# Optimization experiments

Measured on AMD Instinct MI355X. Metric: run time of the kernel, lower is better.

The kernel has to match this reference:

```python
import jax, jax.numpy as jnp
import numpy as np

P = 4  # polynomial kernel degree


def setup_inputs() -> dict:
    key = jax.random.key(0)
    k1, k2, k3, k4 = jax.random.split(key, 4)
    m, n, d = 16384, 8192, 64
    x_p = jax.random.normal(k1, (m, d), dtype=jnp.float32)
    X = jax.random.normal(k2, (n, d), dtype=jnp.float32)
    alpha = jax.random.uniform(k3, (n,), dtype=jnp.float32, minval=0.0, maxval=0.2)
    b = jax.random.uniform(k4, (1,), dtype=jnp.float32, minval=0.0, maxval=0.2)
    return {"x_p": x_p, "X": X, "alpha": alpha, "b": b}


def reference(x_p, X, alpha, b):
    # SVR prediction with polynomial kernel, vectorized:
    # f(x_p) = sum_i alpha_i * (1 + x_p . X_i)^P + b
    # x_p: [m, d], X: [n, d] -> K: [m, n]
    K = (1.0 + jnp.einsum('md,nd->mn', x_p, X)) ** P
    return K @ alpha + b  # [m]
```

## Files before the change

kernel.cpp:

```cpp
#include <hip/hip_runtime.h>
#include <hip/hip_bf16.h>
#include <stdint.h>


typedef __attribute__((ext_vector_type(8))) short bf16x8;
typedef __attribute__((ext_vector_type(8))) unsigned short ushort8;
typedef __attribute__((ext_vector_type(4))) float f32x4;

#define MM 16384
#define NN 8192
#define DD 64
#define NSPLIT 8
#define CHUNK 64
#define CHUNKS_PER_BLK 16
#define BM 128

__device__ __forceinline__ unsigned short f2bf(float f) {
    uint32_t u = __float_as_uint(f);
    uint32_t r = (u + 0x7FFFu + ((u >> 16) & 1u)) >> 16;
    return (unsigned short)r;
}

__device__ __forceinline__ void gll16(const void* g, void* l) {
    __builtin_amdgcn_global_load_lds(
        (const __attribute__((address_space(1))) unsigned int*)g,
        (__attribute__((address_space(3))) unsigned int*)l, 16, 0, 0);
}

__global__ void convert_kernel(const float* __restrict__ xp,
                               const float* __restrict__ X,
                               const float* __restrict__ alpha,
                               unsigned short* __restrict__ xbf,
                               unsigned short* __restrict__ Xs,
                               float* __restrict__ alpha4f) {
    const int xp4 = MM * DD / 4;
    const int xu = NN * DD / 8;
    const int tot = xp4 + xu;
    int tid0 = blockIdx.x * blockDim.x + threadIdx.x;
    if (tid0 < NN) alpha4f[tid0] = sqrtf(sqrtf(alpha[tid0]));
    int stride = gridDim.x * blockDim.x;
    for (int i = tid0; i < tot; i += stride) {
        if (i < xp4) {
            float4 v = ((const float4*)xp)[i];
            ushort4 o;
            o.x = f2bf(v.x); o.y = f2bf(v.y); o.z = f2bf(v.z); o.w = f2bf(v.w);
            *(ushort4*)(xbf + (size_t)i * 4) = o;
        } else {
            int u = i - xp4;
            int n = u >> 3;
            int slot = u & 7;
            float a4 = sqrtf(sqrtf(alpha[n]));
            float4 va = ((const float4*)X)[n * 16 + slot * 2];
            float4 vb = ((const float4*)X)[n * 16 + slot * 2 + 1];
            ushort8 o;
            o[0] = f2bf(va.x * a4); o[1] = f2bf(va.y * a4);
            o[2] = f2bf(va.z * a4); o[3] = f2bf(va.w * a4);
            o[4] = f2bf(vb.x * a4); o[5] = f2bf(vb.y * a4);
            o[6] = f2bf(vb.z * a4); o[7] = f2bf(vb.w * a4);
            size_t dst = (size_t)(n >> 6) * 4096 + (n & 63) * 64
                       + ((slot ^ (n & 7)) * 8);
            *(ushort8*)(Xs + dst) = o;
        }
    }
}

__global__ __launch_bounds__(256) void svr_main(
        const unsigned short* __restrict__ xbf,
        const unsigned short* __restrict__ Xs,
        const float* __restrict__ alpha4f,
        float* __restrict__ partials) {
    __shared__ char smem[16384];
    const int tid  = threadIdx.x;
    const int lane = tid & 63;
    const int w    = tid >> 6;
    const int r    = lane & 15;
    const int g    = lane >> 4;
    const int mgroup = blockIdx.x >> 3;
    const int ns     = blockIdx.x & 7;

    bf16x8 a[2][2];
#pragma unroll
    for (int mt = 0; mt < 2; ++mt)
#pragma unroll
        for (int ks = 0; ks < 2; ++ks)
            a[mt][ks] = *(const bf16x8*)(
                xbf + (size_t)(mgroup * BM + w * 32 + mt * 16 + r) * DD
                    + ks * 32 + g * 8);

    f32x4 red[2];
#pragma unroll
    for (int mt = 0; mt < 2; ++mt) red[mt] = (f32x4){0.f, 0.f, 0.f, 0.f};

    const int chunk0 = ns * CHUNKS_PER_BLK;

    {
        const char* gs = (const char*)Xs + (size_t)chunk0 * 8192 + tid * 16;
        char* lb = smem + w * 1024;
        gll16(gs, lb);
        gll16(gs + 4096, lb + 4096);
    }
    float av4[4];
#pragma unroll
    for (int nt = 0; nt < 4; ++nt)
        av4[nt] = alpha4f[chunk0 * CHUNK + nt * 16 + r];
    __syncthreads();

    int cur = 0;
#pragma unroll 1
    for (int c = 0; c < CHUNKS_PER_BLK; ++c) {
        float av4n[4];
        if (c + 1 < CHUNKS_PER_BLK) {
            const char* gs = (const char*)Xs
                           + (size_t)(chunk0 + c + 1) * 8192 + tid * 16;
            char* lb = smem + (cur ^ 1) * 8192 + w * 1024;
            gll16(gs, lb);
            gll16(gs + 4096, lb + 4096);
#pragma unroll
            for (int nt = 0; nt < 4; ++nt)
                av4n[nt] = alpha4f[(chunk0 + c + 1) * CHUNK + nt * 16 + r];
        }
        bf16x8 b[4][2];
#pragma unroll
        for (int nt = 0; nt < 4; ++nt) {
            const int rr = nt * 16 + r;
            const char* rowp = smem + cur * 8192 + rr * 128;
#pragma unroll
            for (int bh = 0; bh < 2; ++bh) {
                const int slot = (bh * 4 + g) ^ (rr & 7);
                b[nt][bh] = *(const bf16x8*)(rowp + slot * 16);
            }
        }
        f32x4 acc[2][4];
#pragma unroll
        for (int mt = 0; mt < 2; ++mt)
#pragma unroll
            for (int nt = 0; nt < 4; ++nt)
                acc[mt][nt] = (f32x4){av4[nt], av4[nt], av4[nt], av4[nt]};
#pragma unroll
        for (int bh = 0; bh < 2; ++bh)
#pragma unroll
            for (int nt = 0; nt < 4; ++nt)
#pragma unroll
                for (int mt = 0; mt < 2; ++mt)
                    acc[mt][nt] = __builtin_amdgcn_mfma_f32_16x16x32_bf16(
                        a[mt][bh], b[nt][bh], acc[mt][nt], 0, 0, 0);
#pragma unroll
        for (int mt = 0; mt < 2; ++mt)
#pragma unroll
            for (int nt = 0; nt < 4; ++nt)
#pragma unroll
                for (int i = 0; i < 4; ++i) {
                    float t = acc[mt][nt][i];
                    float t2 = t * t;
                    red[mt][i] = fmaf(t2, t2, red[mt][i]);
                }
        __syncthreads();
        cur ^= 1;
        if (c + 1 < CHUNKS_PER_BLK) {
#pragma unroll
            for (int nt = 0; nt < 4; ++nt) av4[nt] = av4n[nt];
        }
    }

#pragma unroll
    for (int mt = 0; mt < 2; ++mt)
#pragma unroll
        for (int i = 0; i < 4; ++i) {
            float v = red[mt][i];
            v += __shfl_xor(v, 1);
            v += __shfl_xor(v, 2);
            v += __shfl_xor(v, 4);
            v += __shfl_xor(v, 8);
            red[mt][i] = v;
        }
    if (r == 0) {
#pragma unroll
        for (int mt = 0; mt < 2; ++mt)
#pragma unroll
            for (int i = 0; i < 4; ++i) {
                int row = mgroup * BM + w * 32 + mt * 16 + g * 4 + i;
                partials[(size_t)ns * MM + row] = red[mt][i];
            }
    }
}

__global__ void finalize_kernel(const float* __restrict__ partials,
                                const float* __restrict__ bbias,
                                float* __restrict__ out) {
    int m = blockIdx.x * blockDim.x + threadIdx.x;
    if (m < MM) {
        float s = bbias[0];
#pragma unroll
        for (int c = 0; c < NSPLIT; ++c) s += partials[(size_t)c * MM + m];
        out[m] = s;
    }
}

extern "C" void kernel_launch(void* const* d_in, const int* in_sizes, int n_in,
                              void* d_out, int out_size, void* d_ws, size_t ws_size,
                              hipStream_t stream) {
    const float* xp    = (const float*)d_in[0];
    const float* X     = (const float*)d_in[1];
    const float* alpha = (const float*)d_in[2];
    const float* b     = (const float*)d_in[3];
    float* out = (float*)d_out;

    unsigned short* xbf = (unsigned short*)d_ws;
    unsigned short* Xs  = xbf + (size_t)MM * DD;
    float* alpha4f = (float*)(Xs + (size_t)NN * DD);
    float* partials = alpha4f + NN;

    hipLaunchKernelGGL(convert_kernel, dim3(1280), dim3(256), 0, stream,
                       xp, X, alpha, xbf, Xs, alpha4f);

    hipLaunchKernelGGL(svr_main, dim3(128 * NSPLIT), dim3(256), 0, stream,
                       xbf, Xs, alpha4f, partials);

    hipLaunchKernelGGL(finalize_kernel, dim3(MM / 256), dim3(256), 0, stream,
                       partials, b, out);
}
```

Baseline: 35.31 us.

## Split waves over N columns instead of M rows, reduce across waves in LDS

Measured after the change: 41.15 us. 16.6% more time.

```diff
diff --git a/kernel.cpp b/kernel.cpp
--- a/kernel.cpp
+++ b/kernel.cpp
@@ -14,6 +14,7 @@
 #define CHUNK 64
 #define CHUNKS_PER_BLK 16
 #define BM 128
+#define MT 8
 
 __device__ __forceinline__ unsigned short f2bf(float f) {
     uint32_t u = __float_as_uint(f);
@@ -78,20 +79,21 @@
     const int mgroup = blockIdx.x >> 3;
     const int ns     = blockIdx.x & 7;
 
-    bf16x8 a[2][2];
-#pragma unroll
-    for (int mt = 0; mt < 2; ++mt)
+    bf16x8 a[MT][2];
+#pragma unroll
+    for (int mt = 0; mt < MT; ++mt)
 #pragma unroll
         for (int ks = 0; ks < 2; ++ks)
             a[mt][ks] = *(const bf16x8*)(
-                xbf + (size_t)(mgroup * BM + w * 32 + mt * 16 + r) * DD
+                xbf + (size_t)(mgroup * BM + mt * 16 + r) * DD
                     + ks * 32 + g * 8);
 
-    f32x4 red[2];
-#pragma unroll
-    for (int mt = 0; mt < 2; ++mt) red[mt] = (f32x4){0.f, 0.f, 0.f, 0.f};
+    f32x4 red[MT];
+#pragma unroll
+    for (int mt = 0; mt < MT; ++mt) red[mt] = (f32x4){0.f, 0.f, 0.f, 0.f};
 
     const int chunk0 = ns * CHUNKS_PER_BLK;
+    const int rr = w * 16 + r;
 
     {
         const char* gs = (const char*)Xs + (size_t)chunk0 * 8192 + tid * 16;
@@ -99,71 +101,49 @@
         gll16(gs, lb);
         gll16(gs + 4096, lb + 4096);
     }
-    float av4[4];
-#pragma unroll
-    for (int nt = 0; nt < 4; ++nt)
-        av4[nt] = alpha4f[chunk0 * CHUNK + nt * 16 + r];
+    float av_cur = alpha4f[chunk0 * CHUNK + rr];
     __syncthreads();
 
     int cur = 0;
 #pragma unroll 1
     for (int c = 0; c < CHUNKS_PER_BLK; ++c) {
-        float av4n[4];
+        float av_nxt;
         if (c + 1 < CHUNKS_PER_BLK) {
             const char* gs = (const char*)Xs
                            + (size_t)(chunk0 + c + 1) * 8192 + tid * 16;
             char* lb = smem + (cur ^ 1) * 8192 + w * 1024;
             gll16(gs, lb);
             gll16(gs + 4096, lb + 4096);
-#pragma unroll
-            for (int nt = 0; nt < 4; ++nt)
-                av4n[nt] = alpha4f[(chunk0 + c + 1) * CHUNK + nt * 16 + r];
+            av_nxt = alpha4f[(chunk0 + c + 1) * CHUNK + rr];
         }
-        bf16x8 b[4][2];
-#pragma unroll
-        for (int nt = 0; nt < 4; ++nt) {
-            const int rr = nt * 16 + r;
-            const char* rowp = smem + cur * 8192 + rr * 128;
-#pragma unroll
-            for (int bh = 0; bh < 2; ++bh) {
-                const int slot = (bh * 4 + g) ^ (rr & 7);
-                b[nt][bh] = *(const bf16x8*)(rowp + slot * 16);
+        const char* rowp = smem + cur * 8192 + rr * 128;
+        bf16x8 b0 = *(const bf16x8*)(rowp + ((g ^ (rr & 7)) * 16));
+        bf16x8 b1 = *(const bf16x8*)(rowp + (((4 + g) ^ (rr & 7)) * 16));
+        f32x4 acc[MT];
+#pragma unroll
+        for (int mt = 0; mt < MT; ++mt)
+            acc[mt] = (f32x4){av_cur, av_cur, av_cur, av_cur};
+#pragma unroll
+        for (int mt = 0; mt < MT; ++mt)
+            acc[mt] = __builtin_amdgcn_mfma_f32_16x16x32_bf16(a[mt][0], b0, acc[mt], 0, 0, 0);
+#pragma unroll
+        for (int mt = 0; mt < MT; ++mt)
+            acc[mt] = __builtin_amdgcn_mfma_f32_16x16x32_bf16(a[mt][1], b1, acc[mt], 0, 0, 0);
+#pragma unroll
+        for (int mt = 0; mt < MT; ++mt)
+#pragma unroll
+            for (int i = 0; i < 4; ++i) {
+                float t = acc[mt][i];
+                float t2 = t * t;
+                red[mt][i] = fmaf(t2, t2, red[mt][i]);
             }
-        }
-        f32x4 acc[2][4];
-#pragma unroll
-        for (int mt = 0; mt < 2; ++mt)
-#pragma unroll
-            for (int nt = 0; nt < 4; ++nt)
-                acc[mt][nt] = (f32x4){av4[nt], av4[nt], av4[nt], av4[nt]};
-#pragma unroll
-        for (int bh = 0; bh < 2; ++bh)
-#pragma unroll
-            for (int nt = 0; nt < 4; ++nt)
-#pragma unroll
-                for (int mt = 0; mt < 2; ++mt)
-                    acc[mt][nt] = __builtin_amdgcn_mfma_f32_16x16x32_bf16(
-                        a[mt][bh], b[nt][bh], acc[mt][nt], 0, 0, 0);
-#pragma unroll
-        for (int mt = 0; mt < 2; ++mt)
-#pragma unroll
-            for (int nt = 0; nt < 4; ++nt)
-#pragma unroll
-                for (int i = 0; i < 4; ++i) {
-                    float t = acc[mt][nt][i];
-                    float t2 = t * t;
-                    red[mt][i] = fmaf(t2, t2, red[mt][i]);
-                }
         __syncthreads();
         cur ^= 1;
-        if (c + 1 < CHUNKS_PER_BLK) {
-#pragma unroll
-            for (int nt = 0; nt < 4; ++nt) av4[nt] = av4n[nt];
-        }
-    }
-
-#pragma unroll
-    for (int mt = 0; mt < 2; ++mt)
+        if (c + 1 < CHUNKS_PER_BLK) av_cur = av_nxt;
+    }
+
+#pragma unroll
+    for (int mt = 0; mt < MT; ++mt)
 #pragma unroll
         for (int i = 0; i < 4; ++i) {
             float v = red[mt][i];
@@ -173,14 +153,19 @@
             v += __shfl_xor(v, 8);
             red[mt][i] = v;
         }
+    float* sred = (float*)smem;
     if (r == 0) {
 #pragma unroll
-        for (int mt = 0; mt < 2; ++mt)
-#pragma unroll
-            for (int i = 0; i < 4; ++i) {
-                int row = mgroup * BM + w * 32 + mt * 16 + g * 4 + i;
-                partials[(size_t)ns * MM + row] = red[mt][i];
-            }
+        for (int mt = 0; mt < MT; ++mt)
+#pragma unroll
+            for (int i = 0; i < 4; ++i)
+                sred[w * BM + mt * 16 + g * 4 + i] = red[mt][i];
+    }
+    __syncthreads();
+    if (tid < BM) {
+        float s = sred[tid] + sred[BM + tid] + sred[2 * BM + tid]
+                + sred[3 * BM + tid];
+        partials[(size_t)ns * MM + mgroup * BM + tid] = s;
     }
 }
 
```
